# Kernel optimization log

Hardware: AMD Instinct MI355X
Metric: run time of the kernel (lower is better)

The kernel has to match this reference:

```python
import jax, jax.numpy as jnp
import numpy as np

SHOTS = 5  # kernel height of all convs; K must equal SHOTS


def _conv2d(x, w, b, stride, pad):
    # x: (N, C, H, W), w: (O, I, kh, kw)
    y = jax.lax.conv_general_dilated(
        x, w, window_strides=stride, padding=pad,
        dimension_numbers=("NCHW", "OIHW", "NCHW"))
    return y + b[None, :, None, None]


def setup_inputs() -> dict:
    key = jax.random.key(0)
    ks = jax.random.split(key, 10)
    B, N, K, D, NQ = 8, 20, SHOTS, 230, 200
    s = 0.05
    return {
        "S": jax.random.normal(ks[0], (B, N, K, D), jnp.float32),
        "Q": jax.random.normal(ks[1], (B, NQ, D), jnp.float32),
        "fc_w": jax.random.normal(ks[2], (D, D), jnp.float32) * s,
        "fc_b": jax.random.normal(ks[3], (D,), jnp.float32) * s,
        "conv1_w": jax.random.normal(ks[4], (32, 1, SHOTS, 1), jnp.float32) * s,
        "conv1_b": jax.random.normal(ks[5], (32,), jnp.float32) * s,
        "conv2_w": jax.random.normal(ks[6], (64, 32, SHOTS, 1), jnp.float32) * s,
        "conv2_b": jax.random.normal(ks[7], (64,), jnp.float32) * s,
        "convf_w": jax.random.normal(ks[8], (1, 64, SHOTS, 1), jnp.float32) * s,
        "convf_b": jax.random.normal(ks[9], (1,), jnp.float32) * s,
    }


def reference(S, Q, fc_w, fc_b, conv1_w, conv1_b, conv2_w, conv2_b, convf_w, convf_b):
    B, N, K, D = S.shape
    NQ = Q.shape[1]
    p = SHOTS // 2

    # ---- conv score extraction over the K (shot) axis ----
    x = S.reshape(B * N, 1, K, D)
    x = jax.nn.relu(_conv2d(x, conv1_w, conv1_b, (1, 1), [(p, p), (0, 0)]))
    x = jax.nn.relu(_conv2d(x, conv2_w, conv2_b, (1, 1), [(p, p), (0, 0)]))
    # dropout is identity in eval mode
    x = jax.nn.relu(_conv2d(x, convf_w, convf_b, (SHOTS, 1), [(0, 0), (0, 0)]))
    score = x.reshape(B, N, D)  # BxNxD

    # ---- hybrid attention prototype ----
    # fc applied to broadcast-expanded tensors == fc applied once, then broadcast
    Sf = S @ fc_w.T + fc_b            # B x N x K x D
    Qf = Q @ fc_w.T + fc_b            # B x NQ x D
    if K == 1:
        S_repre = jnp.broadcast_to(S.mean(-2)[:, None], (B, NQ, N, D))
    else:
        # tanh(S_fc * Q_fc).sum(-1) -> softmax over K
        t = jnp.tanh(Sf[:, None, :, :, :] * Qf[:, :, None, None, :])  # B,NQ,N,K,D
        att = jax.nn.softmax(t.sum(-1), axis=-1)                      # B,NQ,N,K
        S_repre = jnp.einsum("bqnk,bnkd->bqnd", att, S)               # B,NQ,N,D

    # ---- weighted squared L2 distance ----
    diff = S_repre - Q[:, :, None, :]                                  # B,NQ,N,D
    logits = -jnp.sum(diff * diff * score[:, None, :, :] * 700.0, axis=-1)  # B,NQ,N
    return (logits, S)
```

## Files before the change

kernel.cpp:

```cpp
#include <hip/hip_runtime.h>
#include <hip/hip_bf16.h>

typedef _Float16 f16x8 __attribute__((ext_vector_type(8)));
typedef float f32x4 __attribute__((ext_vector_type(4)));

#define BB 8
#define NN 20
#define KK 5
#define DD 230
#define NQ 200
#define QST 256

#define NB_BFC 240
#define NB_BP  200
#define NB_CONV 575
#define NB_FC2 38
#define NB_ATT 800
#define NB_CP 90

static __device__ __forceinline__ unsigned int pk2(float a, float b) {
    union { __fp16 h[2] __attribute__((aligned(4))); unsigned int u; } v;
    v.h[0] = (__fp16)a; v.h[1] = (__fp16)b; return v.u;
}

__global__ void k_pre(const float* __restrict__ fc_w,
                      const float* __restrict__ w2, const float* __restrict__ b2,
                      const float* __restrict__ wf,
                      _Float16* __restrict__ Bfc, _Float16* __restrict__ Bp,
                      float2* __restrict__ tblg) {
    const int bid = blockIdx.x, tid = threadIdx.x;
    if (bid < NB_BFC) {
        int g = bid * 256 + tid;
        int kg = g & 31;
        int ncl = (g >> 5) & 15;
        int tk = g >> 9;
        int nt = tk >> 3, ks = tk & 7;
        int n = nt * 16 + ncl, k = ks * 32 + kg;
        float val = (n < DD && k < DD) ? fc_w[n * DD + k] : 0.f;
        Bfc[g] = (_Float16)val;
    } else {
        int g = (bid - NB_BFC) * 256 + tid;
        int kg = g & 31;
        int ncl = (g >> 5) & 15;
        int tk = g >> 9;
        int nt = tk / 5, ks = tk - nt * 5;
        int n = nt * 16 + ncl, k = ks * 32 + kg;
        int o = n / 5, i = n % 5;
        int c = k / 5, j = k - c * 5;
        int t = j - i + 2;
        float val = (t >= 0 && t < 5) ? w2[(o * 32 + c) * 5 + t] : 0.f;
        Bp[g] = (_Float16)val;
        if (g < 320) {
            int o2 = g / 5, i2 = g % 5;
            tblg[g] = make_float2(b2[o2], wf[o2 * 5 + i2]);
        }
    }
}

__global__ __launch_bounds__(512)
void k_main(const float* __restrict__ S, const float* __restrict__ Q,
            const float* __restrict__ w1, const float* __restrict__ b1,
            const _Float16* __restrict__ Bp, const _Float16* __restrict__ Bfc,
            const float2* __restrict__ tblg, float* __restrict__ sc,
            const float* __restrict__ fc_b,
            float* __restrict__ Sf, float* __restrict__ Qf) {
    __shared__ __align__(16) _Float16 XU[64 * 264];
    __shared__ float xfp[8][16];
    const int bid = blockIdx.x, tid = threadIdx.x;
    const int lane = tid & 63;
    const int w = __builtin_amdgcn_readfirstlane(tid >> 6);
    const int ncl = lane & 15;
    const int kg8 = (lane >> 4) * 8;
    const int g4 = lane >> 4;

    if (bid >= NB_CONV) {
        const int m0 = (bid - NB_CONV) * 64;
        for (int e = tid; e < 64 * 58; e += 512) {
            int row = e / 58, c4 = e - row * 58;
            int grow = m0 + row;
            float4 v = make_float4(0.f, 0.f, 0.f, 0.f);
            if (grow < 2400) {
                const float* inp = (grow < 800) ? S + (size_t)grow * DD
                                                : Q + (size_t)(grow - 800) * DD;
                if (c4 < 57) v = *(const float4*)&inp[c4 * 4];
                else { v.x = inp[228]; v.y = inp[229]; }
            }
            _Float16* xp = &XU[row * 264 + c4 * 4];
            xp[0] = (_Float16)v.x; xp[1] = (_Float16)v.y;
            xp[2] = (_Float16)v.z; xp[3] = (_Float16)v.w;
        }
        for (int e = tid; e < 64 * 16; e += 512) {
            int row = e >> 4, cc = 232 + (e & 15) * 2;
            *(unsigned int*)&XU[row * 264 + cc] = 0u;
        }
        __syncthreads();

        const int msub = w & 3;
        const int ngrp = w >> 2;
        f16x8 af[8];
#pragma unroll
        for (int ks = 0; ks < 8; ks++)
            af[ks] = *(const f16x8*)&XU[(msub * 16 + ncl) * 264 + ks * 32 + kg8];

        const int nt0 = ngrp * 8;
        const int ntn = ngrp ? 7 : 8;
        for (int ti = 0; ti < ntn; ti++) {
            const int nt = nt0 + ti;
            const _Float16* bp = Bfc + ((size_t)nt * 8 * 16) * 32;
            f32x4 a = {0.f, 0.f, 0.f, 0.f};
#pragma unroll
            for (int ks = 0; ks < 8; ks++) {
                f16x8 br = *(const f16x8*)&bp[(ks * 16 + ncl) * 32 + kg8];
                a = __builtin_amdgcn_mfma_f32_16x16x32_f16(af[ks], br, a, 0, 0, 0);
            }
            const int n = nt * 16 + ncl;
            const float bias = fc_b[n < DD ? n : DD - 1];
            if (n < DD) {
#pragma unroll
                for (int r = 0; r < 4; r++) {
                    int grow = m0 + msub * 16 + g4 * 4 + r;
                    if (grow < 800)
                        Sf[(size_t)grow * DD + n] = (a[r] + bias) * 2.8853900817779268f;
                    else if (grow < 2400)
                        Qf[(size_t)(grow - 800) * QST + n] = a[r] + bias;
                }
            }
        }
        return;
    }

    const int m0 = bid * 64;
    {
        const int m = m0 + lane;
        const int img = m / DD;
        const int d = m - img * DD;
        const float* sp = S + (size_t)img * KK * DD + d;
        float in5[5];
#pragma unroll
        for (int j = 0; j < 5; j++) in5[j] = sp[j * DD];
#pragma unroll
        for (int cc = 0; cc < 4; cc++) {
            int c = w * 4 + cc;
            float wl[5];
#pragma unroll
            for (int t = 0; t < 5; t++) wl[t] = w1[c * 5 + t];
            float bb = b1[c];
#pragma unroll
            for (int i = 0; i < 5; i++) {
                float a = bb;
#pragma unroll
                for (int t = 0; t < 5; t++) {
                    int j = i + t - 2;
                    if (j >= 0 && j < 5) a = fmaf(wl[t], in5[j], a);
                }
                XU[lane * 168 + c * 5 + i] = (_Float16)fmaxf(a, 0.f);
            }
        }
    }
    __syncthreads();

    const int msub = w & 3;
    const int gq = w >> 2;
    f16x8 af[5];
#pragma unroll
    for (int ks = 0; ks < 5; ks++)
        af[ks] = *(const f16x8*)&XU[(msub * 16 + ncl) * 168 + ks * 32 + kg8];

    float xf = 0.f;
#pragma unroll 2
    for (int t10 = 0; t10 < 10; t10++) {
        const int nt = gq * 10 + t10;
        const _Float16* bp = Bp + ((size_t)nt * 5 * 16) * 32;
        f32x4 a = {0.f, 0.f, 0.f, 0.f};
#pragma unroll
        for (int ks = 0; ks < 5; ks++) {
            f16x8 br = *(const f16x8*)&bp[(ks * 16 + ncl) * 32 + kg8];
            a = __builtin_amdgcn_mfma_f32_16x16x32_f16(br, af[ks], a, 0, 0, 0);
        }
        float2 tb[4];
#pragma unroll
        for (int r = 0; r < 4; r++) tb[r] = tblg[nt * 16 + g4 * 4 + r];
#pragma unroll
        for (int r = 0; r < 4; r++)
            xf = fmaf(fmaxf(a[r] + tb[r].x, 0.f), tb[r].y, xf);
    }
    xf += __shfl_xor(xf, 16, 64);
    xf += __shfl_xor(xf, 32, 64);
    if (lane < 16) xfp[w][lane] = xf;
    __syncthreads();
    if (tid < 64) {
        const int ms = tid >> 4, j = tid & 15;
        sc[m0 + ms * 16 + j] = xfp[ms][j] + xfp[ms + 4][j];
    }
}

__global__ __launch_bounds__(512)
void k_att(const float* __restrict__ Sf, const float* __restrict__ Qf,
           const float* __restrict__ S, const float* __restrict__ Q,
           const float* __restrict__ sc, const float* __restrict__ convf_b,
           float* __restrict__ out, float* __restrict__ Scopy) {
    __shared__ __align__(16) _Float16 SfT[32 * 264];
    __shared__ __align__(16) float Lw[8][32];
    const int bid = blockIdx.x, tid = threadIdx.x;
    if (bid >= NB_ATT) {
        int g = (bid - NB_ATT) * 512 + tid;
        if (g < 46000) ((float4*)Scopy)[g] = ((const float4*)S)[g];
        return;
    }
    const int lane = tid & 63;
    const int w = __builtin_amdgcn_readfirstlane(tid >> 6);
    const int b = bid / 100;
    const int nq = (bid / 25) & 3;
    const int qg = bid % 25;
    const int q = qg * 8 + w;
    const int n0 = nq * 5;
    const int ncl = lane & 15;
    const int g4 = lane >> 4;
    const int kg8 = g4 * 8;
    const float LOG2E = 1.4426950408889634f;
    const float bf0 = convf_b[0];

    const float* sfb = Sf + (size_t)(b * 100 + n0 * 5) * DD;
    for (int e = tid; e < 32 * 132; e += 512) {
        int row = e / 132, c2 = e - row * 132;
        unsigned int u = 0u;
        if (row < 25 && c2 <= 114) {
            float2 v = *(const float2*)&sfb[row * DD + 2 * c2];
            u = pk2(v.x, v.y);
        }
        *(unsigned int*)&SfT[row * 264 + 2 * c2] = u;
    }
    __syncthreads();

    f16x8 ones;
#pragma unroll
    for (int j = 0; j < 8; j++) ones[j] = (_Float16)1.f;
    f32x4 acc0 = {0.f, 0.f, 0.f, 0.f}, acc1 = {0.f, 0.f, 0.f, 0.f};

    const float* qfp = Qf + (size_t)(b * NQ + q) * QST;
    for (int ks = 0; ks < 8; ks++) {
        f32x4 qa = *(const f32x4*)&qfp[ks * 32 + kg8];
        f32x4 qb = *(const f32x4*)&qfp[ks * 32 + kg8 + 4];
        float qv[8];
#pragma unroll
        for (int j = 0; j < 4; j++) { qv[j] = qa[j]; qv[4 + j] = qb[j]; }
#pragma unroll
        for (int t = 0; t < 2; t++) {
            f16x8 s8 = *(const f16x8*)&SfT[(t * 16 + ncl) * 264 + ks * 32 + kg8];
            f16x8 vf;
#pragma unroll
            for (int j = 0; j < 8; j++) {
                float x = (float)s8[j] * qv[j];
                float e = __builtin_amdgcn_exp2f(x);
                float v = 1.f - 2.f * __builtin_amdgcn_rcpf(e + 1.f);
                vf[j] = (_Float16)v;
            }
            if (t == 0) acc0 = __builtin_amdgcn_mfma_f32_16x16x32_f16(vf, ones, acc0, 0, 0, 0);
            else        acc1 = __builtin_amdgcn_mfma_f32_16x16x32_f16(vf, ones, acc1, 0, 0, 0);
        }
    }
    if (ncl == 0) {
        *(f32x4*)&Lw[w][g4 * 4] = acc0;
        *(f32x4*)&Lw[w][16 + g4 * 4] = acc1;
    }

    float qr[4];
    const float* qp = Q + (size_t)(b * NQ + q) * DD;
#pragma unroll
    for (int i = 0; i < 4; i++) {
        int d = lane + 64 * i;
        qr[i] = (d < DD) ? qp[d] : 0.f;
    }
    for (int nl = 0; nl < 5; nl++) {
        const float* lp = &Lw[w][nl * 5];
        float v0 = lp[0], v1 = lp[1], v2 = lp[2], v3 = lp[3], v4 = lp[4];
        float m = fmaxf(fmaxf(fmaxf(v0, v1), fmaxf(v2, v3)), v4);
        float e0 = __builtin_amdgcn_exp2f((v0 - m) * LOG2E);
        float e1 = __builtin_amdgcn_exp2f((v1 - m) * LOG2E);
        float e2 = __builtin_amdgcn_exp2f((v2 - m) * LOG2E);
        float e3 = __builtin_amdgcn_exp2f((v3 - m) * LOG2E);
        float e4 = __builtin_amdgcn_exp2f((v4 - m) * LOG2E);
        float inv = __builtin_amdgcn_rcpf(e0 + e1 + e2 + e3 + e4);
        float a0 = e0 * inv, a1 = e1 * inv, a2 = e2 * inv, a3 = e3 * inv, a4 = e4 * inv;
        const int n = n0 + nl;
        const float* spn = S + (size_t)(b * NN + n) * KK * DD;
        const float* s0 = sc + (size_t)(b * NN + n) * DD;
        float acc2 = 0.f;
#pragma unroll
        for (int i = 0; i < 4; i++) {
            int d = lane + 64 * i;
            if (d < DD) {
                float rep = a0 * spn[d] + a1 * spn[DD + d] + a2 * spn[2 * DD + d]
                          + a3 * spn[3 * DD + d] + a4 * spn[4 * DD + d];
                float df = rep - qr[i];
                float scw = fmaxf(s0[d] + bf0, 0.f) * 700.f;
                acc2 = fmaf(df * df, scw, acc2);
            }
        }
#pragma unroll
        for (int off = 32; off > 0; off >>= 1) acc2 += __shfl_xor(acc2, off, 64);
        if (lane == 0) out[((size_t)b * NQ + q) * NN + n] = -acc2;
    }
}

extern "C" void kernel_launch(void* const* d_in, const int* in_sizes, int n_in,
                              void* d_out, int out_size, void* d_ws, size_t ws_size,
                              hipStream_t stream) {
    const float* S       = (const float*)d_in[0];
    const float* Q       = (const float*)d_in[1];
    const float* fc_w    = (const float*)d_in[2];
    const float* fc_b    = (const float*)d_in[3];
    const float* conv1_w = (const float*)d_in[4];
    const float* conv1_b = (const float*)d_in[5];
    const float* conv2_w = (const float*)d_in[6];
    const float* conv2_b = (const float*)d_in[7];
    const float* convf_w = (const float*)d_in[8];
    const float* convf_b = (const float*)d_in[9];
    float* out = (float*)d_out;

    float* ws = (float*)d_ws;
    float* Sf  = ws;
    float* Qf  = Sf + 184000;
    float* sc  = Qf + 409600;
    _Float16* Bp  = (_Float16*)(sc + 36800);
    _Float16* Bfc = Bp + 51200;
    float2* tblg  = (float2*)(Bfc + 61440);

    k_pre<<<NB_BFC + NB_BP, 256, 0, stream>>>(
        fc_w, conv2_w, conv2_b, convf_w, Bfc, Bp, tblg);
    k_main<<<NB_CONV + NB_FC2, 512, 0, stream>>>(
        S, Q, conv1_w, conv1_b, Bp, Bfc, tblg, sc, fc_b, Sf, Qf);
    k_att<<<NB_ATT + NB_CP, 512, 0, stream>>>(
        Sf, Qf, S, Q, sc, convf_b, out, out + (size_t)BB * NQ * NN);
}
```

Before: 67.77 us.

## Move S copy into prep kernel, reuse B fragments across two M-strips, stage Qf in LDS

The S pass-through copy moves from extra blocks of the attention kernel into the prep kernel, with the block count adjusted for 256-thread blocks. In the conv MFMA stage each wave now covers two 16-row strips and five N-tiles instead of one strip and ten, so each loaded Bp fragment feeds two MFMAs. The final reduction sums four partials per output. The attention kernel stages the block's 8 Qf rows in shared memory instead of reading them per wave from global, at the cost of extra LDS and one more fill loop before the barrier.

```diff
diff --git a/kernel.cpp b/kernel.cpp
--- a/kernel.cpp
+++ b/kernel.cpp
@@ -13,10 +13,10 @@
 
 #define NB_BFC 240
 #define NB_BP  200
+#define NB_CP  180
 #define NB_CONV 575
 #define NB_FC2 38
 #define NB_ATT 800
-#define NB_CP 90
 
 static __device__ __forceinline__ unsigned int pk2(float a, float b) {
     union { __fp16 h[2] __attribute__((aligned(4))); unsigned int u; } v;
@@ -27,7 +27,8 @@
                       const float* __restrict__ w2, const float* __restrict__ b2,
                       const float* __restrict__ wf,
                       _Float16* __restrict__ Bfc, _Float16* __restrict__ Bp,
-                      float2* __restrict__ tblg) {
+                      float2* __restrict__ tblg,
+                      const float* __restrict__ S, float* __restrict__ Scopy) {
     const int bid = blockIdx.x, tid = threadIdx.x;
     if (bid < NB_BFC) {
         int g = bid * 256 + tid;
@@ -38,7 +39,7 @@
         int n = nt * 16 + ncl, k = ks * 32 + kg;
         float val = (n < DD && k < DD) ? fc_w[n * DD + k] : 0.f;
         Bfc[g] = (_Float16)val;
-    } else {
+    } else if (bid < NB_BFC + NB_BP) {
         int g = (bid - NB_BFC) * 256 + tid;
         int kg = g & 31;
         int ncl = (g >> 5) & 15;
@@ -54,6 +55,9 @@
             int o2 = g / 5, i2 = g % 5;
             tblg[g] = make_float2(b2[o2], wf[o2 * 5 + i2]);
         }
+    } else {
+        int g = (bid - NB_BFC - NB_BP) * 256 + tid;
+        if (g < 46000) ((float4*)Scopy)[g] = ((const float4*)S)[g];
     }
 }
 
@@ -65,7 +69,7 @@
             const float* __restrict__ fc_b,
             float* __restrict__ Sf, float* __restrict__ Qf) {
     __shared__ __align__(16) _Float16 XU[64 * 264];
-    __shared__ float xfp[8][16];
+    __shared__ float xfp[8][2][16];
     const int bid = blockIdx.x, tid = threadIdx.x;
     const int lane = tid & 63;
     const int w = __builtin_amdgcn_readfirstlane(tid >> 6);
@@ -159,38 +163,49 @@
     }
     __syncthreads();
 
-    const int msub = w & 3;
-    const int gq = w >> 2;
-    f16x8 af[5];
-#pragma unroll
-    for (int ks = 0; ks < 5; ks++)
-        af[ks] = *(const f16x8*)&XU[(msub * 16 + ncl) * 168 + ks * 32 + kg8];
-
-    float xf = 0.f;
-#pragma unroll 2
-    for (int t10 = 0; t10 < 10; t10++) {
-        const int nt = gq * 10 + t10;
+    const int mh = w & 1;
+    const int gq = w >> 1;
+    f16x8 af0[5], af1[5];
+#pragma unroll
+    for (int ks = 0; ks < 5; ks++) {
+        af0[ks] = *(const f16x8*)&XU[((mh * 2 + 0) * 16 + ncl) * 168 + ks * 32 + kg8];
+        af1[ks] = *(const f16x8*)&XU[((mh * 2 + 1) * 16 + ncl) * 168 + ks * 32 + kg8];
+    }
+
+    float xf0 = 0.f, xf1 = 0.f;
+#pragma unroll
+    for (int t5 = 0; t5 < 5; t5++) {
+        const int nt = gq * 5 + t5;
         const _Float16* bp = Bp + ((size_t)nt * 5 * 16) * 32;
-        f32x4 a = {0.f, 0.f, 0.f, 0.f};
+        f16x8 br[5];
+#pragma unroll
+        for (int ks = 0; ks < 5; ks++)
+            br[ks] = *(const f16x8*)&bp[(ks * 16 + ncl) * 32 + kg8];
+        f32x4 a0 = {0.f, 0.f, 0.f, 0.f}, a1 = {0.f, 0.f, 0.f, 0.f};
 #pragma unroll
         for (int ks = 0; ks < 5; ks++) {
-            f16x8 br = *(const f16x8*)&bp[(ks * 16 + ncl) * 32 + kg8];
-            a = __builtin_amdgcn_mfma_f32_16x16x32_f16(br, af[ks], a, 0, 0, 0);
+            a0 = __builtin_amdgcn_mfma_f32_16x16x32_f16(br[ks], af0[ks], a0, 0, 0, 0);
+            a1 = __builtin_amdgcn_mfma_f32_16x16x32_f16(br[ks], af1[ks], a1, 0, 0, 0);
         }
         float2 tb[4];
 #pragma unroll
         for (int r = 0; r < 4; r++) tb[r] = tblg[nt * 16 + g4 * 4 + r];
 #pragma unroll
-        for (int r = 0; r < 4; r++)
-            xf = fmaf(fmaxf(a[r] + tb[r].x, 0.f), tb[r].y, xf);
-    }
-    xf += __shfl_xor(xf, 16, 64);
-    xf += __shfl_xor(xf, 32, 64);
-    if (lane < 16) xfp[w][lane] = xf;
+        for (int r = 0; r < 4; r++) {
+            xf0 = fmaf(fmaxf(a0[r] + tb[r].x, 0.f), tb[r].y, xf0);
+            xf1 = fmaf(fmaxf(a1[r] + tb[r].x, 0.f), tb[r].y, xf1);
+        }
+    }
+    xf0 += __shfl_xor(xf0, 16, 64); xf0 += __shfl_xor(xf0, 32, 64);
+    xf1 += __shfl_xor(xf1, 16, 64); xf1 += __shfl_xor(xf1, 32, 64);
+    if (lane < 16) { xfp[w][0][lane] = xf0; xfp[w][1][lane] = xf1; }
     __syncthreads();
     if (tid < 64) {
-        const int ms = tid >> 4, j = tid & 15;
-        sc[m0 + ms * 16 + j] = xfp[ms][j] + xfp[ms + 4][j];
+        const int strip = tid >> 4, col = tid & 15;
+        const int mhh = strip >> 1, idx = strip & 1;
+        float s = xfp[mhh][idx][col] + xfp[mhh + 2][idx][col]
+                + xfp[mhh + 4][idx][col] + xfp[mhh + 6][idx][col];
+        sc[m0 + strip * 16 + col] = s;
     }
 }
 
@@ -198,15 +213,11 @@
 void k_att(const float* __restrict__ Sf, const float* __restrict__ Qf,
            const float* __restrict__ S, const float* __restrict__ Q,
            const float* __restrict__ sc, const float* __restrict__ convf_b,
-           float* __restrict__ out, float* __restrict__ Scopy) {
+           float* __restrict__ out) {
     __shared__ __align__(16) _Float16 SfT[32 * 264];
     __shared__ __align__(16) float Lw[8][32];
+    __shared__ __align__(16) float Qs[8][256];
     const int bid = blockIdx.x, tid = threadIdx.x;
-    if (bid >= NB_ATT) {
-        int g = (bid - NB_ATT) * 512 + tid;
-        if (g < 46000) ((float4*)Scopy)[g] = ((const float4*)S)[g];
-        return;
-    }
     const int lane = tid & 63;
     const int w = __builtin_amdgcn_readfirstlane(tid >> 6);
     const int b = bid / 100;
@@ -230,6 +241,12 @@
         }
         *(unsigned int*)&SfT[row * 264 + 2 * c2] = u;
     }
+    for (int e = tid; e < 8 * 256; e += 512) {
+        int row = e >> 8, col = e & 255;
+        float v = 0.f;
+        if (col < DD) v = Qf[(size_t)(b * NQ + qg * 8 + row) * QST + col];
+        Qs[row][col] = v;
+    }
     __syncthreads();
 
     f16x8 ones;
@@ -237,10 +254,9 @@
     for (int j = 0; j < 8; j++) ones[j] = (_Float16)1.f;
     f32x4 acc0 = {0.f, 0.f, 0.f, 0.f}, acc1 = {0.f, 0.f, 0.f, 0.f};
 
-    const float* qfp = Qf + (size_t)(b * NQ + q) * QST;
     for (int ks = 0; ks < 8; ks++) {
-        f32x4 qa = *(const f32x4*)&qfp[ks * 32 + kg8];
-        f32x4 qb = *(const f32x4*)&qfp[ks * 32 + kg8 + 4];
+        f32x4 qa = *(const f32x4*)&Qs[w][ks * 32 + kg8];
+        f32x4 qb = *(const f32x4*)&Qs[w][ks * 32 + kg8 + 4];
         float qv[8];
 #pragma unroll
         for (int j = 0; j < 4; j++) { qv[j] = qa[j]; qv[4 + j] = qb[j]; }
@@ -326,10 +342,11 @@
     _Float16* Bfc = Bp + 51200;
     float2* tblg  = (float2*)(Bfc + 61440);
 
-    k_pre<<<NB_BFC + NB_BP, 256, 0, stream>>>(
-        fc_w, conv2_w, conv2_b, convf_w, Bfc, Bp, tblg);
+    k_pre<<<NB_BFC + NB_BP + NB_CP, 256, 0, stream>>>(
+        fc_w, conv2_w, conv2_b, convf_w, Bfc, Bp, tblg,
+        S, out + (size_t)BB * NQ * NN);
     k_main<<<NB_CONV + NB_FC2, 512, 0, stream>>>(
         S, Q, conv1_w, conv1_b, Bp, Bfc, tblg, sc, fc_b, Sf, Qf);
-    k_att<<<NB_ATT + NB_CP, 512, 0, stream>>>(
-        Sf, Qf, S, Q, sc, convf_b, out, out + (size_t)BB * NQ * NN);
-}
+    k_att<<<NB_ATT, 512, 0, stream>>>(
+        Sf, Qf, S, Q, sc, convf_b, out);
+}
```

New measurement: 64.49 us. -4.8%, faster.
